# Performance work log

Hardware: AMD Instinct MI355X
Metric: run time of the kernel (lower is better)

Reference implementation:

```python
import jax, jax.numpy as jnp
import numpy as np

B, T, D = 4, 2048, 1024

def setup_inputs() -> dict:
    key = jax.random.key(0)
    kx, kq, kk, kv = jax.random.split(key, 4)
    return {
        "vector": jax.random.normal(kx, (B, T, D), dtype=jnp.float32),
        # original uses torch.rand -> uniform [0,1)
        "W_queries": jax.random.uniform(kq, (D, D), dtype=jnp.float32),
        "W_keys": jax.random.uniform(kk, (D, D), dtype=jnp.float32),
        "W_values": jax.random.uniform(kv, (D, D), dtype=jnp.float32),
    }

def reference(vector, W_queries, W_keys, W_values):
    b, num_token, d_out = vector.shape
    queries = vector @ W_queries          # [b, t, d]
    keys = vector @ W_keys                # [b, t, d]
    values = vector @ W_values            # [b, t, d]
    # attention_score: [b, q, k]
    scores = jnp.einsum('bqd,bkd->bqk', queries, keys)
    causal_mask = jnp.triu(jnp.ones((num_token, num_token), dtype=bool), k=1)
    scores = jnp.where(causal_mask[None, :, :], -jnp.inf, scores)
    # NOTE: original uses FLOOR division `//` by sqrt(d_k) -- faithful here.
    inv_sqrt_scale = jnp.asarray(np.sqrt(keys.shape[-1]), dtype=scores.dtype)
    weights = jnp.floor(scores / inv_sqrt_scale)
    # NOTE: original applies softmax over dim=1 (the query axis), not dim=-1.
    weights = jax.nn.softmax(weights, axis=1)
    # dropout rate is 0.0 (eval/deterministic): identity
    context = jnp.einsum('bqk,bkd->bqd', weights, values)
    return context
```

## Files before the change

kernel.cpp:

```cpp
#include <hip/hip_runtime.h>
#include <math.h>

typedef _Float16 half4 __attribute__((ext_vector_type(4)));
typedef _Float16 half8 __attribute__((ext_vector_type(8)));
typedef float f32x4 __attribute__((ext_vector_type(4)));

#define GLD16(gptr, lptr)                                                     \
    __builtin_amdgcn_global_load_lds(                                         \
        (const __attribute__((address_space(1))) unsigned int*)(gptr),        \
        (__attribute__((address_space(3))) unsigned int*)(lptr), 16, 0, 0)

#define WAIT_VM(N) asm volatile("s_waitcnt vmcnt(" #N ")" ::: "memory")
#define BARRIER()  __builtin_amdgcn_s_barrier()
#define SCHED_FENCE() __builtin_amdgcn_sched_barrier(0)

namespace {

constexpr int Bb = 4;
constexpr int Tt = 2048;
constexpr int Dd = 1024;
constexpr int BT = Bb * Tt;
constexpr int NCH = 16;

__device__ inline _Float16 f2h(float f) { return (_Float16)f; }

__global__ __launch_bounds__(256) void convert_x_kernel(
    const float* __restrict__ X, _Float16* __restrict__ Xhi, _Float16* __restrict__ Xlo)
{
    const int idx = (blockIdx.x * 256 + threadIdx.x) * 4;
    const float4 v = *(const float4*)(X + idx);
    const float a[4] = {v.x, v.y, v.z, v.w};
    half4 h, l;
#pragma unroll
    for (int i = 0; i < 4; ++i) {
        h[i] = f2h(a[i]);
        l[i] = f2h(a[i] - (float)h[i]);
    }
    *(half4*)(Xhi + idx) = h;
    *(half4*)(Xlo + idx) = l;
}

__global__ __launch_bounds__(256) void convert_wqk_kernel(
    const float* __restrict__ Wq, const float* __restrict__ Wk,
    _Float16* __restrict__ Wqh, _Float16* __restrict__ Wql,
    _Float16* __restrict__ Wkh, _Float16* __restrict__ Wkl)
{
    const int mat = blockIdx.y;
    const float* W = mat ? Wk : Wq;
    _Float16* Hh = mat ? Wkh : Wqh;
    _Float16* Ll = mat ? Wkl : Wql;
    const int idx = (blockIdx.x * 256 + threadIdx.x) * 4;
    const float4 v = *(const float4*)(W + idx);
    const float a[4] = {v.x, v.y, v.z, v.w};
    half4 h, l;
#pragma unroll
    for (int i = 0; i < 4; ++i) {
        h[i] = f2h(a[i]);
        l[i] = f2h(a[i] - (float)h[i]);
    }
    *(half4*)(Hh + idx) = h;
    *(half4*)(Ll + idx) = l;
}

__global__ __launch_bounds__(256) void convert_wv_kernel(
    const float* __restrict__ Wv, _Float16* __restrict__ WvTh)
{
    __shared__ float tile[64][65];
    const int n0 = blockIdx.x * 64, k0 = blockIdx.y * 64;
    const int tx = threadIdx.x & 63, ty = threadIdx.x >> 6;
#pragma unroll
    for (int i = 0; i < 16; ++i)
        tile[ty + i * 4][tx] = Wv[(size_t)(k0 + ty + i * 4) * Dd + n0 + tx];
    __syncthreads();
#pragma unroll
    for (int i = 0; i < 16; ++i) {
        const float v = tile[tx][ty + i * 4];
        WvTh[(size_t)(n0 + ty + i * 4) * Dd + k0 + tx] = f2h(v);
    }
}

__global__ __launch_bounds__(256) void gt_kernel(
    const _Float16* __restrict__ Wkh, const _Float16* __restrict__ Wkl,
    const _Float16* __restrict__ Wqh, const _Float16* __restrict__ Wql,
    _Float16* __restrict__ GTh, _Float16* __restrict__ GTl)
{
    __shared__ _Float16 Ahl[2][2][4][512];
    __shared__ _Float16 Bhl[2][2][4][512];

    const int n0 = blockIdx.x * 64;
    const int m0 = blockIdx.y * 64;
    const int tid = threadIdx.x;
    const int w = tid >> 6, lane = tid & 63;
    const int lr = lane & 15, lq = lane >> 4;
    const int wi = (w >> 1) * 2, wj = (w & 1) * 2;

    f32x4 acc[2][2];
#pragma unroll
    for (int i = 0; i < 2; ++i)
#pragma unroll
        for (int j = 0; j < 2; ++j)
#pragma unroll
            for (int c = 0; c < 4; ++c) acc[i][j][c] = 0.f;

    auto stage = [&](int bf, int kk) {
        const int s = w;
        const size_t ar = (size_t)(m0 + s * 16 + lr) * Dd + kk + lq * 8;
        const size_t br = (size_t)(n0 + s * 16 + lr) * Dd + kk + lq * 8;
        GLD16(Wkh + ar, &Ahl[bf][0][s][0]);
        GLD16(Wkl + ar, &Ahl[bf][1][s][0]);
        GLD16(Wqh + br, &Bhl[bf][0][s][0]);
        GLD16(Wql + br, &Bhl[bf][1][s][0]);
    };

    stage(0, 0);
    int ib = 0;
    for (int step = 0; step < 32; ++step, ib ^= 1) {
        if (step < 31) {
            stage(ib ^ 1, (step + 1) << 5);
            WAIT_VM(4);
        } else {
            WAIT_VM(0);
        }
        BARRIER();
        SCHED_FENCE();
        half8 ah[2], al[2], bh[2], bl[2];
#pragma unroll
        for (int i = 0; i < 2; ++i) {
            ah[i] = *(const half8*)&Ahl[ib][0][wi + i][lane * 8];
            al[i] = *(const half8*)&Ahl[ib][1][wi + i][lane * 8];
        }
#pragma unroll
        for (int j = 0; j < 2; ++j) {
            bh[j] = *(const half8*)&Bhl[ib][0][wj + j][lane * 8];
            bl[j] = *(const half8*)&Bhl[ib][1][wj + j][lane * 8];
        }
#pragma unroll
        for (int i = 0; i < 2; ++i)
#pragma unroll
            for (int j = 0; j < 2; ++j) {
                acc[i][j] = __builtin_amdgcn_mfma_f32_16x16x32_f16(ah[i], bh[j], acc[i][j], 0, 0, 0);
                acc[i][j] = __builtin_amdgcn_mfma_f32_16x16x32_f16(ah[i], bl[j], acc[i][j], 0, 0, 0);
                acc[i][j] = __builtin_amdgcn_mfma_f32_16x16x32_f16(al[i], bh[j], acc[i][j], 0, 0, 0);
            }
        BARRIER();
    }

#pragma unroll
    for (int i = 0; i < 2; ++i)
#pragma unroll
        for (int r = 0; r < 4; ++r) {
            const int row = m0 + (wi + i) * 16 + lq * 4 + r;
#pragma unroll
            for (int j = 0; j < 2; ++j) {
                const int col = n0 + (wj + j) * 16 + lr;
                const float v = acc[i][j][r];
                const _Float16 h = f2h(v);
                GTh[(size_t)row * Dd + col] = h;
                GTl[(size_t)row * Dd + col] = f2h(v - (float)h);
            }
        }
}

__global__ __launch_bounds__(256, 2) void tv_kernel(
    const _Float16* __restrict__ Xhi, const _Float16* __restrict__ Xlo,
    const _Float16* __restrict__ GTh, const _Float16* __restrict__ GTl,
    const _Float16* __restrict__ WvTh,
    _Float16* __restrict__ Thi, _Float16* __restrict__ Tlo,
    _Float16* __restrict__ Vt)
{
    __shared__ _Float16 smem[32768];
    auto A_ = [&](int bf, int hl, int s) -> _Float16* {
        return smem + ((bf * 2 + hl) * 8 + s) * 512;
    };
    auto B_ = [&](int bf, int hl, int s) -> _Float16* {
        return smem + 16384 + ((bf * 2 + hl) * 8 + s) * 512;
    };

    const int f  = blockIdx.x;
    const int fp = (f & 7) * 128 + (f >> 3);
    const int mb  = fp >> 4;
    const int sub = fp & 15;
    const int m0 = mb * 128;
    const int n0 = (sub & 7) * 128;

    const int tid = threadIdx.x;
    const int w = tid >> 6, lane = tid & 63;
    const int lr = lane & 15, lq = lane >> 4;
    const int wr = (w >> 1) * 4, wc = (w & 1) * 4;

    f32x4 acc[4][4];
#pragma unroll
    for (int i = 0; i < 4; ++i)
#pragma unroll
        for (int j = 0; j < 4; ++j)
#pragma unroll
            for (int c = 0; c < 4; ++c) acc[i][j][c] = 0.f;

    if (sub < 8) {
        auto stage = [&](int bf, int kk) {
#pragma unroll
            for (int s2 = 0; s2 < 2; ++s2) {
                const int s = w * 2 + s2;
                const size_t ar = (size_t)(m0 + s * 16 + lr) * Dd + kk + lq * 8;
                const size_t br = (size_t)(n0 + s * 16 + lr) * Dd + kk + lq * 8;
                GLD16(Xhi + ar, A_(bf, 0, s));
                GLD16(Xlo + ar, A_(bf, 1, s));
                GLD16(GTh + br, B_(bf, 0, s));
                GLD16(GTl + br, B_(bf, 1, s));
            }
        };
        stage(0, 0);
        int ib = 0;
        for (int step = 0; step < 32; ++step, ib ^= 1) {
            if (step < 31) {
                stage(ib ^ 1, (step + 1) << 5);
                WAIT_VM(8);
            } else {
                WAIT_VM(0);
            }
            BARRIER();
            SCHED_FENCE();
            half8 ah[4], al[4], bh[4], bl[4];
#pragma unroll
            for (int i = 0; i < 4; ++i) {
                ah[i] = *(const half8*)(A_(ib, 0, wr + i) + lane * 8);
                al[i] = *(const half8*)(A_(ib, 1, wr + i) + lane * 8);
            }
#pragma unroll
            for (int j = 0; j < 4; ++j) {
                bh[j] = *(const half8*)(B_(ib, 0, wc + j) + lane * 8);
                bl[j] = *(const half8*)(B_(ib, 1, wc + j) + lane * 8);
            }
#pragma unroll
            for (int i = 0; i < 4; ++i)
#pragma unroll
                for (int j = 0; j < 4; ++j) {
                    acc[i][j] = __builtin_amdgcn_mfma_f32_16x16x32_f16(ah[i], bh[j], acc[i][j], 0, 0, 0);
                    acc[i][j] = __builtin_amdgcn_mfma_f32_16x16x32_f16(ah[i], bl[j], acc[i][j], 0, 0, 0);
                    acc[i][j] = __builtin_amdgcn_mfma_f32_16x16x32_f16(al[i], bh[j], acc[i][j], 0, 0, 0);
                }
            BARRIER();
        }
#pragma unroll
        for (int i = 0; i < 4; ++i)
#pragma unroll
            for (int r = 0; r < 4; ++r) {
                const int row = m0 + (wr + i) * 16 + lq * 4 + r;
#pragma unroll
                for (int j = 0; j < 4; ++j) {
                    const int col = n0 + (wc + j) * 16 + lr;
                    const float v = acc[i][j][r];
                    const _Float16 h = f2h(v);
                    Thi[(size_t)row * Dd + col] = h;
                    Tlo[(size_t)row * Dd + col] = f2h(v - (float)h);
                }
            }
    } else {
        auto stage = [&](int bf, int kk) {
#pragma unroll
            for (int s2 = 0; s2 < 2; ++s2) {
                const int s = w * 2 + s2;
                GLD16(Xhi + (size_t)(m0 + s * 16 + lr) * Dd + kk + lq * 8, A_(bf, 0, s));
                GLD16(WvTh + (size_t)(n0 + s * 16 + lr) * Dd + kk + lq * 8, B_(bf, 0, s));
            }
        };
        stage(0, 0);
        int ib = 0;
        for (int step = 0; step < 32; ++step, ib ^= 1) {
            if (step < 31) {
                stage(ib ^ 1, (step + 1) << 5);
                WAIT_VM(4);
            } else {
                WAIT_VM(0);
            }
            BARRIER();
            SCHED_FENCE();
            half8 a[4], b2[4];
#pragma unroll
            for (int i = 0; i < 4; ++i) a[i] = *(const half8*)(A_(ib, 0, wr + i) + lane * 8);
#pragma unroll
            for (int j = 0; j < 4; ++j) b2[j] = *(const half8*)(B_(ib, 0, wc + j) + lane * 8);
#pragma unroll
            for (int i = 0; i < 4; ++i)
#pragma unroll
                for (int j = 0; j < 4; ++j)
                    acc[i][j] = __builtin_amdgcn_mfma_f32_16x16x32_f16(a[i], b2[j], acc[i][j], 0, 0, 0);
            BARRIER();
        }
        __syncthreads();
#pragma unroll
        for (int i = 0; i < 4; ++i)
#pragma unroll
            for (int r2 = 0; r2 < 4; ++r2) {
                const int rloc = (wr + i) * 16 + lq * 4 + r2;
#pragma unroll
                for (int j = 0; j < 4; ++j) {
                    const int cloc = (wc + j) * 16 + lr;
                    smem[cloc * 136 + rloc] = f2h(acc[i][j][r2]);
                }
            }
        __syncthreads();
        const int b2i = m0 >> 11;
        const int t0  = m0 & 2047;
        const int dloc = tid >> 1, tl = (tid & 1) * 64;
        _Float16* vp = Vt + (size_t)b2i * Dd * Tt + (size_t)(n0 + dloc) * Tt + t0 + tl;
#pragma unroll
        for (int e = 0; e < 8; ++e)
            *(half8*)(vp + e * 8) = *(const half8*)&smem[dloc * 136 + tl + e * 8];
    }
}

__global__ __launch_bounds__(256, 2) void scores_mfma_kernel(
    const _Float16* __restrict__ Thi, const _Float16* __restrict__ Tlo,
    const _Float16* __restrict__ Xhi, const _Float16* __restrict__ Xlo,
    float* __restrict__ S, float* __restrict__ Pm, float* __restrict__ Pl)
{
    const int f  = blockIdx.x;
    const int fp = (f & 7) * 68 + (f >> 3);
    const int b = fp / 136;
    const int t = fp - b * 136;
    int byi = (int)((sqrtf(8.f * t + 1.f) - 1.f) * 0.5f);
    if ((byi + 1) * (byi + 2) / 2 <= t) ++byi;
    if (byi * (byi + 1) / 2 > t) --byi;
    const int bxi = t - byi * (byi + 1) / 2;
    const int j0 = bxi * 128, q0 = byi * 128;
    float* Sb = S + (size_t)b * Tt * Tt;

    __shared__ _Float16 Ahl[2][2][8][512];
    __shared__ _Float16 Bhl[2][2][8][512];
    const _Float16* Th = Thi + (size_t)b * Tt * Dd;
    const _Float16* Tl = Tlo + (size_t)b * Tt * Dd;
    const _Float16* Xh = Xhi + (size_t)b * Tt * Dd;
    const _Float16* Xl = Xlo + (size_t)b * Tt * Dd;

    const int tid = threadIdx.x;
    const int w = tid >> 6, lane = tid & 63;
    const int lr = lane & 15, lq = lane >> 4;
    const int wr = (w >> 1) * 4, wc = (w & 1) * 4;

    f32x4 acc[4][4];
#pragma unroll
    for (int i = 0; i < 4; ++i)
#pragma unroll
        for (int j = 0; j < 4; ++j)
#pragma unroll
            for (int c = 0; c < 4; ++c) acc[i][j][c] = 0.f;

    auto stage = [&](int bf, int kk) {
#pragma unroll
        for (int s2 = 0; s2 < 2; ++s2) {
            const int s = w * 2 + s2;
            const size_t ar = (size_t)(q0 + s * 16 + lr) * Dd + kk + lq * 8;
            const size_t br = (size_t)(j0 + s * 16 + lr) * Dd + kk + lq * 8;
            GLD16(Th + ar, &Ahl[bf][0][s][0]);
            GLD16(Tl + ar, &Ahl[bf][1][s][0]);
            GLD16(Xh + br, &Bhl[bf][0][s][0]);
            GLD16(Xl + br, &Bhl[bf][1][s][0]);
        }
    };

    stage(0, 0);
    int ib = 0;
    for (int step = 0; step < 32; ++step, ib ^= 1) {
        if (step < 31) {
            stage(ib ^ 1, (step + 1) << 5);
            WAIT_VM(8);
        } else {
            WAIT_VM(0);
        }
        BARRIER();
        SCHED_FENCE();
        half8 ah[4], al[4], bh[4], bl[4];
#pragma unroll
        for (int i = 0; i < 4; ++i) {
            ah[i] = *(const half8*)&Ahl[ib][0][wr + i][lane * 8];
            al[i] = *(const half8*)&Ahl[ib][1][wr + i][lane * 8];
        }
#pragma unroll
        for (int j = 0; j < 4; ++j) {
            bh[j] = *(const half8*)&Bhl[ib][0][wc + j][lane * 8];
            bl[j] = *(const half8*)&Bhl[ib][1][wc + j][lane * 8];
        }
#pragma unroll
        for (int i = 0; i < 4; ++i)
#pragma unroll
            for (int j = 0; j < 4; ++j) {
                acc[i][j] = __builtin_amdgcn_mfma_f32_16x16x32_f16(ah[i], bh[j], acc[i][j], 0, 0, 0);
                acc[i][j] = __builtin_amdgcn_mfma_f32_16x16x32_f16(ah[i], bl[j], acc[i][j], 0, 0, 0);
                acc[i][j] = __builtin_amdgcn_mfma_f32_16x16x32_f16(al[i], bh[j], acc[i][j], 0, 0, 0);
            }
        BARRIER();
    }

    float sv[4][4][4];
#pragma unroll
    for (int i = 0; i < 4; ++i)
#pragma unroll
        for (int r = 0; r < 4; ++r) {
            const int q = q0 + (wr + i) * 16 + lq * 4 + r;
#pragma unroll
            for (int j = 0; j < 4; ++j) {
                const int jg = j0 + (wc + j) * 16 + lr;
                const float v = (jg <= q) ? floorf(acc[i][j][r] * 0.03125f) : -INFINITY;
                sv[i][j][r] = v;
                Sb[(size_t)q * Tt + jg] = v;
            }
        }

    float* red  = (float*)&Ahl[0][0][0][0];
    float* colm = red + 2048;
    __syncthreads();
    for (int e = tid; e < 2048; e += 256) red[e] = -INFINITY;
    __syncthreads();
    const int rowidx = (w * 4 + lq) * 128;
#pragma unroll
    for (int j = 0; j < 4; ++j) {
        const int c = (wc + j) * 16 + lr;
        float lm = -INFINITY;
#pragma unroll
        for (int i = 0; i < 4; ++i)
#pragma unroll
            for (int r = 0; r < 4; ++r) lm = fmaxf(lm, sv[i][j][r]);
        red[rowidx + c] = lm;
    }
    __syncthreads();
    if (tid < 128) {
        float m = -INFINITY;
#pragma unroll
        for (int e = 0; e < 16; ++e) m = fmaxf(m, red[e * 128 + tid]);
        colm[tid] = m;
    }
    __syncthreads();
    float ls[4];
#pragma unroll
    for (int j = 0; j < 4; ++j) {
        const int c = (wc + j) * 16 + lr;
        const float m = colm[c];
        float s = 0.f;
#pragma unroll
        for (int i = 0; i < 4; ++i)
#pragma unroll
            for (int r = 0; r < 4; ++r)
                if (sv[i][j][r] != -INFINITY) s += __expf(sv[i][j][r] - m);
        ls[j] = s;
    }
    __syncthreads();
    for (int e = tid; e < 2048; e += 256) red[e] = 0.f;
    __syncthreads();
#pragma unroll
    for (int j = 0; j < 4; ++j) red[rowidx + (wc + j) * 16 + lr] = ls[j];
    __syncthreads();
    if (tid < 128) {
        float l = 0.f;
#pragma unroll
        for (int e = 0; e < 16; ++e) l += red[e * 128 + tid];
        const size_t o = ((size_t)b * NCH + byi) * Tt + j0 + tid;
        Pm[o] = colm[tid];
        Pl[o] = l;
    }
}

__global__ __launch_bounds__(256) void colstats_merge_kernel(
    const float* __restrict__ Pm, const float* __restrict__ Pl,
    float* __restrict__ Mb, float* __restrict__ Lb)
{
    const int j = blockIdx.x * 256 + threadIdx.x;
    const int b = blockIdx.y;
    const int jt = j >> 7;
    float m = -INFINITY, l = 0.f;
    for (int c = jt; c < NCH; ++c) {
        const size_t pidx = ((size_t)b * NCH + c) * Tt + j;
        const float mi = Pm[pidx];
        if (mi == -INFINITY) continue;
        const float li = Pl[pidx];
        if (mi > m) { l = l * __expf(m - mi) + li; m = mi; }
        else        { l += li * __expf(mi - m); }
    }
    Mb[(size_t)b * Tt + j] = m;
    Lb[(size_t)b * Tt + j] = (l > 0.f) ? 1.f / l : 0.f;
}

__global__ __launch_bounds__(256) void context_mfma_kernel(
    const float* __restrict__ S, const float* __restrict__ Mb,
    const float* __restrict__ Lb, const _Float16* __restrict__ Vt,
    float* __restrict__ Out)
{
    __shared__ _Float16 As[8][512];
    __shared__ _Float16 Bl[2][8][512];

    const int f  = blockIdx.x;
    const int fp = (f & 7) * 64 + (f >> 3);
    const int b  = fp >> 7;
    const int r  = fp & 127;
    const int bx = r & 7;
    const int tq = r >> 3;
    const int by = (tq & 1) ? (15 - (tq >> 1)) : (tq >> 1);
    const int d0 = bx * 128;
    const int q0 = by * 128;
    const float* Sb = S + (size_t)b * Tt * Tt;
    const float* Mp = Mb + (size_t)b * Tt;
    const float* Lp = Lb + (size_t)b * Tt;
    const _Float16* Vb = Vt + (size_t)b * Dd * Tt;
    float* Ob = Out + (size_t)b * Tt * Dd;

    const int tid = threadIdx.x;
    const int w = tid >> 6, lane = tid & 63;
    const int lr = lane & 15, lq = lane >> 4;
    const int wr = (w >> 1) * 4, wc = (w & 1) * 4;

    f32x4 acc[4][4];
#pragma unroll
    for (int i = 0; i < 4; ++i)
#pragma unroll
        for (int j = 0; j < 4; ++j)
#pragma unroll
            for (int c = 0; c < 4; ++c) acc[i][j][c] = 0.f;

    float4 sreg[4];
    float4 mreg[2], lreg[2];

    auto issue = [&](int ib2, int k0) {
        const int kc = k0 + lq * 8;
#pragma unroll
        for (int s2 = 0; s2 < 2; ++s2) {
            const int s = w * 2 + s2;
            const float* sp = Sb + (size_t)(q0 + s * 16 + lr) * Tt + kc;
            sreg[s2 * 2]     = *(const float4*)sp;
            sreg[s2 * 2 + 1] = *(const float4*)(sp + 4);
        }
        mreg[0] = *(const float4*)(Mp + kc);
        mreg[1] = *(const float4*)(Mp + kc + 4);
        lreg[0] = *(const float4*)(Lp + kc);
        lreg[1] = *(const float4*)(Lp + kc + 4);
#pragma unroll
        for (int s2 = 0; s2 < 2; ++s2) {
            const int s = w * 2 + s2;
            GLD16(Vb + (size_t)(d0 + s * 16 + lr) * Tt + k0 + lq * 8, &Bl[ib2][s][0]);
        }
    };
    auto writeA = [&]() {
        const float mm[8] = {mreg[0].x, mreg[0].y, mreg[0].z, mreg[0].w,
                             mreg[1].x, mreg[1].y, mreg[1].z, mreg[1].w};
        const float ll[8] = {lreg[0].x, lreg[0].y, lreg[0].z, lreg[0].w,
                             lreg[1].x, lreg[1].y, lreg[1].z, lreg[1].w};
#pragma unroll
        for (int s2 = 0; s2 < 2; ++s2) {
            const int s = w * 2 + s2;
            const float4 s0 = sreg[s2 * 2], s1 = sreg[s2 * 2 + 1];
            const float sa[8] = {s0.x, s0.y, s0.z, s0.w, s1.x, s1.y, s1.z, s1.w};
            half8 out;
#pragma unroll
            for (int e = 0; e < 8; ++e)
                out[e] = f2h(__expf(sa[e] - mm[e]) * ll[e]);
            *(half8*)&As[s][lane * 8] = out;
        }
    };

    const int nstep = (q0 + 128) >> 5;
    issue(0, 0);
    writeA();
    __syncthreads();
    int ib = 0;
    for (int step = 0; step < nstep; ++step, ib ^= 1) {
        const bool more = (step + 1 < nstep);
        if (more) issue(ib ^ 1, (step + 1) << 5);
        half8 a[4], b2[4];
#pragma unroll
        for (int i = 0; i < 4; ++i) a[i] = *(const half8*)&As[wr + i][lane * 8];
#pragma unroll
        for (int j = 0; j < 4; ++j) b2[j] = *(const half8*)&Bl[ib][wc + j][lane * 8];
#pragma unroll
        for (int i = 0; i < 4; ++i)
#pragma unroll
            for (int j = 0; j < 4; ++j)
                acc[i][j] = __builtin_amdgcn_mfma_f32_16x16x32_f16(a[i], b2[j], acc[i][j], 0, 0, 0);
        if (more) {
            __syncthreads();
            writeA();
            __syncthreads();
        }
    }

#pragma unroll
    for (int i = 0; i < 4; ++i)
#pragma unroll
        for (int r2 = 0; r2 < 4; ++r2) {
            const int row = q0 + (wr + i) * 16 + lq * 4 + r2;
#pragma unroll
            for (int j = 0; j < 4; ++j)
                Ob[(size_t)row * Dd + d0 + (wc + j) * 16 + lr] = acc[i][j][r2];
        }
}

}

extern "C" void kernel_launch(void* const* d_in, const int* in_sizes, int n_in,
                              void* d_out, int out_size, void* d_ws, size_t ws_size,
                              hipStream_t stream)
{
    const float* X  = (const float*)d_in[0];
    const float* Wq = (const float*)d_in[1];
    const float* Wk = (const float*)d_in[2];
    const float* Wv = (const float*)d_in[3];

    char* ws = (char*)d_ws;
    const size_t MB = 1024 * 1024;
    _Float16* Xhi  = (_Float16*)ws;
    _Float16* Xlo  = (_Float16*)(ws + 16 * MB);
    _Float16* Wqh  = (_Float16*)(ws + 32 * MB);
    _Float16* Wql  = (_Float16*)(ws + 34 * MB);
    _Float16* Wkh  = (_Float16*)(ws + 36 * MB);
    _Float16* Wkl  = (_Float16*)(ws + 38 * MB);
    _Float16* WvTh = (_Float16*)(ws + 40 * MB);
    _Float16* GTh  = (_Float16*)(ws + 44 * MB);
    _Float16* GTl  = (_Float16*)(ws + 46 * MB);
    _Float16* Thi  = (_Float16*)(ws + 48 * MB);
    _Float16* Tlo  = (_Float16*)(ws + 64 * MB);
    _Float16* Vt   = (_Float16*)(ws + 80 * MB);
    float*    S    = (float*)(ws + 112 * MB);
    float*    Mb   = (float*)(ws + 176 * MB);
    float*    Lb   = Mb + (size_t)Bb * Tt;
    float*    Pm   = Lb + (size_t)Bb * Tt;
    float*    Pl   = Pm + (size_t)Bb * NCH * Tt;
    float*    Out  = (float*)d_out;

    convert_x_kernel<<<BT * Dd / 1024, 256, 0, stream>>>(X, Xhi, Xlo);
    convert_wqk_kernel<<<dim3(Dd * Dd / 1024, 2), 256, 0, stream>>>(Wq, Wk, Wqh, Wql, Wkh, Wkl);
    convert_wv_kernel<<<dim3(16, 16), 256, 0, stream>>>(Wv, WvTh);
    gt_kernel<<<dim3(16, 16), 256, 0, stream>>>(Wkh, Wkl, Wqh, Wql, GTh, GTl);
    tv_kernel<<<dim3(1024), 256, 0, stream>>>(Xhi, Xlo, GTh, GTl, WvTh, Thi, Tlo, Vt);
    scores_mfma_kernel<<<dim3(544), 256, 0, stream>>>(Thi, Tlo, Xhi, Xlo, S, Pm, Pl);
    colstats_merge_kernel<<<dim3(Tt / 256, Bb), 256, 0, stream>>>(Pm, Pl, Mb, Lb);
    context_mfma_kernel<<<dim3(512), 256, 0, stream>>>(S, Mb, Lb, Vt, Out);
}
```

Baseline: 469.7 us.

## Store tile-local exp probabilities as fp16 and fuse conversion kernels

The scores kernel now writes exp(s - tile column max) as fp16 instead of the raw fp32 scores. The context kernel rescales these using a per-column factor exp(Pm - M) * (1/L), precomputed into shared memory, instead of recomputing exp from fp32 scores. This halves the intermediate matrix traffic and removes exp work from the context loop. The three conversion kernels are also merged into one launch. The risk is extra fp16 rounding of the unnormalized probabilities, and the loop barrier placement changes.

```diff
diff --git a/kernel.cpp b/kernel.cpp
--- a/kernel.cpp
+++ b/kernel.cpp
@@ -24,58 +24,58 @@
 
 __device__ inline _Float16 f2h(float f) { return (_Float16)f; }
 
-__global__ __launch_bounds__(256) void convert_x_kernel(
-    const float* __restrict__ X, _Float16* __restrict__ Xhi, _Float16* __restrict__ Xlo)
-{
-    const int idx = (blockIdx.x * 256 + threadIdx.x) * 4;
-    const float4 v = *(const float4*)(X + idx);
-    const float a[4] = {v.x, v.y, v.z, v.w};
-    half4 h, l;
-#pragma unroll
-    for (int i = 0; i < 4; ++i) {
-        h[i] = f2h(a[i]);
-        l[i] = f2h(a[i] - (float)h[i]);
-    }
-    *(half4*)(Xhi + idx) = h;
-    *(half4*)(Xlo + idx) = l;
-}
-
-__global__ __launch_bounds__(256) void convert_wqk_kernel(
-    const float* __restrict__ Wq, const float* __restrict__ Wk,
+__global__ __launch_bounds__(256) void convert_all_kernel(
+    const float* __restrict__ X,  const float* __restrict__ Wq,
+    const float* __restrict__ Wk, const float* __restrict__ Wv,
+    _Float16* __restrict__ Xhi, _Float16* __restrict__ Xlo,
     _Float16* __restrict__ Wqh, _Float16* __restrict__ Wql,
-    _Float16* __restrict__ Wkh, _Float16* __restrict__ Wkl)
-{
-    const int mat = blockIdx.y;
-    const float* W = mat ? Wk : Wq;
-    _Float16* Hh = mat ? Wkh : Wqh;
-    _Float16* Ll = mat ? Wkl : Wql;
-    const int idx = (blockIdx.x * 256 + threadIdx.x) * 4;
-    const float4 v = *(const float4*)(W + idx);
-    const float a[4] = {v.x, v.y, v.z, v.w};
-    half4 h, l;
-#pragma unroll
-    for (int i = 0; i < 4; ++i) {
-        h[i] = f2h(a[i]);
-        l[i] = f2h(a[i] - (float)h[i]);
-    }
-    *(half4*)(Hh + idx) = h;
-    *(half4*)(Ll + idx) = l;
-}
-
-__global__ __launch_bounds__(256) void convert_wv_kernel(
-    const float* __restrict__ Wv, _Float16* __restrict__ WvTh)
+    _Float16* __restrict__ Wkh, _Float16* __restrict__ Wkl,
+    _Float16* __restrict__ WvTh)
 {
     __shared__ float tile[64][65];
-    const int n0 = blockIdx.x * 64, k0 = blockIdx.y * 64;
-    const int tx = threadIdx.x & 63, ty = threadIdx.x >> 6;
-#pragma unroll
-    for (int i = 0; i < 16; ++i)
-        tile[ty + i * 4][tx] = Wv[(size_t)(k0 + ty + i * 4) * Dd + n0 + tx];
-    __syncthreads();
-#pragma unroll
-    for (int i = 0; i < 16; ++i) {
-        const float v = tile[tx][ty + i * 4];
-        WvTh[(size_t)(n0 + ty + i * 4) * Dd + k0 + tx] = f2h(v);
+    const int f = blockIdx.x;
+    if (f < 8192) {
+        const int idx = f * 1024 + threadIdx.x * 4;
+        const float4 v = *(const float4*)(X + idx);
+        const float a[4] = {v.x, v.y, v.z, v.w};
+        half4 h, l;
+#pragma unroll
+        for (int i = 0; i < 4; ++i) {
+            h[i] = f2h(a[i]);
+            l[i] = f2h(a[i] - (float)h[i]);
+        }
+        *(half4*)(Xhi + idx) = h;
+        *(half4*)(Xlo + idx) = l;
+    } else if (f < 10240) {
+        const int g = f - 8192;
+        const int mat = g >> 10;
+        const float* W = mat ? Wk : Wq;
+        _Float16* Hh = mat ? Wkh : Wqh;
+        _Float16* Ll = mat ? Wkl : Wql;
+        const int idx = (g & 1023) * 1024 + threadIdx.x * 4;
+        const float4 v = *(const float4*)(W + idx);
+        const float a[4] = {v.x, v.y, v.z, v.w};
+        half4 h, l;
+#pragma unroll
+        for (int i = 0; i < 4; ++i) {
+            h[i] = f2h(a[i]);
+            l[i] = f2h(a[i] - (float)h[i]);
+        }
+        *(half4*)(Hh + idx) = h;
+        *(half4*)(Ll + idx) = l;
+    } else {
+        const int g = f - 10240;
+        const int n0 = (g & 15) * 64, k0 = (g >> 4) * 64;
+        const int tx = threadIdx.x & 63, ty = threadIdx.x >> 6;
+#pragma unroll
+        for (int i = 0; i < 16; ++i)
+            tile[ty + i * 4][tx] = Wv[(size_t)(k0 + ty + i * 4) * Dd + n0 + tx];
+        __syncthreads();
+#pragma unroll
+        for (int i = 0; i < 16; ++i) {
+            const float v = tile[tx][ty + i * 4];
+            WvTh[(size_t)(n0 + ty + i * 4) * Dd + k0 + tx] = f2h(v);
+        }
     }
 }
 
@@ -313,7 +313,7 @@
 __global__ __launch_bounds__(256, 2) void scores_mfma_kernel(
     const _Float16* __restrict__ Thi, const _Float16* __restrict__ Tlo,
     const _Float16* __restrict__ Xhi, const _Float16* __restrict__ Xlo,
-    float* __restrict__ S, float* __restrict__ Pm, float* __restrict__ Pl)
+    _Float16* __restrict__ Pp, float* __restrict__ Pm, float* __restrict__ Pl)
 {
     const int f  = blockIdx.x;
     const int fp = (f & 7) * 68 + (f >> 3);
@@ -324,7 +324,7 @@
     if (byi * (byi + 1) / 2 > t) --byi;
     const int bxi = t - byi * (byi + 1) / 2;
     const int j0 = bxi * 128, q0 = byi * 128;
-    float* Sb = S + (size_t)b * Tt * Tt;
+    _Float16* Pb = Pp + (size_t)b * Tt * Tt;
 
     __shared__ _Float16 Ahl[2][2][8][512];
     __shared__ _Float16 Bhl[2][2][8][512];
@@ -401,9 +401,7 @@
 #pragma unroll
             for (int j = 0; j < 4; ++j) {
                 const int jg = j0 + (wc + j) * 16 + lr;
-                const float v = (jg <= q) ? floorf(acc[i][j][r] * 0.03125f) : -INFINITY;
-                sv[i][j][r] = v;
-                Sb[(size_t)q * Tt + jg] = v;
+                sv[i][j][r] = (jg <= q) ? floorf(acc[i][j][r] * 0.03125f) : -INFINITY;
             }
         }
 
@@ -435,13 +433,18 @@
 #pragma unroll
     for (int j = 0; j < 4; ++j) {
         const int c = (wc + j) * 16 + lr;
+        const int jg = j0 + c;
         const float m = colm[c];
         float s = 0.f;
 #pragma unroll
         for (int i = 0; i < 4; ++i)
 #pragma unroll
-            for (int r = 0; r < 4; ++r)
-                if (sv[i][j][r] != -INFINITY) s += __expf(sv[i][j][r] - m);
+            for (int r = 0; r < 4; ++r) {
+                const float e = __expf(sv[i][j][r] - m);
+                s += e;
+                const int q = q0 + (wr + i) * 16 + lq * 4 + r;
+                Pb[(size_t)q * Tt + jg] = f2h(e);
+            }
         ls[j] = s;
     }
     __syncthreads();
@@ -481,12 +484,13 @@
 }
 
 __global__ __launch_bounds__(256) void context_mfma_kernel(
-    const float* __restrict__ S, const float* __restrict__ Mb,
-    const float* __restrict__ Lb, const _Float16* __restrict__ Vt,
-    float* __restrict__ Out)
+    const _Float16* __restrict__ Pp, const float* __restrict__ Pm,
+    const float* __restrict__ Mb, const float* __restrict__ Lb,
+    const _Float16* __restrict__ Vt, float* __restrict__ Out)
 {
     __shared__ _Float16 As[8][512];
     __shared__ _Float16 Bl[2][8][512];
+    __shared__ float cbuf[2048];
 
     const int f  = blockIdx.x;
     const int fp = (f & 7) * 64 + (f >> 3);
@@ -497,7 +501,8 @@
     const int by = (tq & 1) ? (15 - (tq >> 1)) : (tq >> 1);
     const int d0 = bx * 128;
     const int q0 = by * 128;
-    const float* Sb = S + (size_t)b * Tt * Tt;
+    const _Float16* Pb = Pp + (size_t)b * Tt * Tt;
+    const float* Pmb = Pm + ((size_t)b * NCH + by) * Tt;
     const float* Mp = Mb + (size_t)b * Tt;
     const float* Lp = Lb + (size_t)b * Tt;
     const _Float16* Vb = Vt + (size_t)b * Dd * Tt;
@@ -507,6 +512,10 @@
     const int w = tid >> 6, lane = tid & 63;
     const int lr = lane & 15, lq = lane >> 4;
     const int wr = (w >> 1) * 4, wc = (w & 1) * 4;
+    const int kmax = q0 + 128;
+
+    for (int k = tid; k < kmax; k += 256)
+        cbuf[k] = __expf(Pmb[k] - Mp[k]) * Lp[k];
 
     f32x4 acc[4][4];
 #pragma unroll
@@ -516,54 +525,50 @@
 #pragma unroll
             for (int c = 0; c < 4; ++c) acc[i][j][c] = 0.f;
 
-    float4 sreg[4];
-    float4 mreg[2], lreg[2];
-
-    auto issue = [&](int ib2, int k0) {
-        const int kc = k0 + lq * 8;
+    half8 areg[2];
+    auto loadA = [&](int k0) {
 #pragma unroll
         for (int s2 = 0; s2 < 2; ++s2) {
             const int s = w * 2 + s2;
-            const float* sp = Sb + (size_t)(q0 + s * 16 + lr) * Tt + kc;
-            sreg[s2 * 2]     = *(const float4*)sp;
-            sreg[s2 * 2 + 1] = *(const float4*)(sp + 4);
-        }
-        mreg[0] = *(const float4*)(Mp + kc);
-        mreg[1] = *(const float4*)(Mp + kc + 4);
-        lreg[0] = *(const float4*)(Lp + kc);
-        lreg[1] = *(const float4*)(Lp + kc + 4);
+            areg[s2] = *(const half8*)(Pb + (size_t)(q0 + s * 16 + lr) * Tt + k0 + lq * 8);
+        }
+    };
+    auto issueV = [&](int ib2, int k0) {
 #pragma unroll
         for (int s2 = 0; s2 < 2; ++s2) {
             const int s = w * 2 + s2;
             GLD16(Vb + (size_t)(d0 + s * 16 + lr) * Tt + k0 + lq * 8, &Bl[ib2][s][0]);
         }
     };
-    auto writeA = [&]() {
-        const float mm[8] = {mreg[0].x, mreg[0].y, mreg[0].z, mreg[0].w,
-                             mreg[1].x, mreg[1].y, mreg[1].z, mreg[1].w};
-        const float ll[8] = {lreg[0].x, lreg[0].y, lreg[0].z, lreg[0].w,
-                             lreg[1].x, lreg[1].y, lreg[1].z, lreg[1].w};
+    auto writeA = [&](int k0) {
+        const float* cp = cbuf + k0 + lq * 8;
+        float cv[8];
+#pragma unroll
+        for (int e = 0; e < 8; ++e) cv[e] = cp[e];
 #pragma unroll
         for (int s2 = 0; s2 < 2; ++s2) {
             const int s = w * 2 + s2;
-            const float4 s0 = sreg[s2 * 2], s1 = sreg[s2 * 2 + 1];
-            const float sa[8] = {s0.x, s0.y, s0.z, s0.w, s1.x, s1.y, s1.z, s1.w};
             half8 out;
 #pragma unroll
-            for (int e = 0; e < 8; ++e)
-                out[e] = f2h(__expf(sa[e] - mm[e]) * ll[e]);
+            for (int e = 0; e < 8; ++e) out[e] = f2h((float)areg[s2][e] * cv[e]);
             *(half8*)&As[s][lane * 8] = out;
         }
     };
 
-    const int nstep = (q0 + 128) >> 5;
-    issue(0, 0);
-    writeA();
-    __syncthreads();
+    __syncthreads();
+    loadA(0);
+    issueV(0, 0);
+    writeA(0);
+    __syncthreads();
+
     int ib = 0;
+    const int nstep = kmax >> 5;
     for (int step = 0; step < nstep; ++step, ib ^= 1) {
         const bool more = (step + 1 < nstep);
-        if (more) issue(ib ^ 1, (step + 1) << 5);
+        if (more) {
+            loadA((step + 1) << 5);
+            issueV(ib ^ 1, (step + 1) << 5);
+        }
         half8 a[4], b2[4];
 #pragma unroll
         for (int i = 0; i < 4; ++i) a[i] = *(const half8*)&As[wr + i][lane * 8];
@@ -574,9 +579,10 @@
 #pragma unroll
             for (int j = 0; j < 4; ++j)
                 acc[i][j] = __builtin_amdgcn_mfma_f32_16x16x32_f16(a[i], b2[j], acc[i][j], 0, 0, 0);
+        BARRIER();
+        SCHED_FENCE();
         if (more) {
-            __syncthreads();
-            writeA();
+            writeA((step + 1) << 5);
             __syncthreads();
         }
     }
@@ -617,19 +623,18 @@
     _Float16* Thi  = (_Float16*)(ws + 48 * MB);
     _Float16* Tlo  = (_Float16*)(ws + 64 * MB);
     _Float16* Vt   = (_Float16*)(ws + 80 * MB);
-    float*    S    = (float*)(ws + 112 * MB);
+    _Float16* Pp   = (_Float16*)(ws + 112 * MB);
     float*    Mb   = (float*)(ws + 176 * MB);
     float*    Lb   = Mb + (size_t)Bb * Tt;
     float*    Pm   = Lb + (size_t)Bb * Tt;
     float*    Pl   = Pm + (size_t)Bb * NCH * Tt;
     float*    Out  = (float*)d_out;
 
-    convert_x_kernel<<<BT * Dd / 1024, 256, 0, stream>>>(X, Xhi, Xlo);
-    convert_wqk_kernel<<<dim3(Dd * Dd / 1024, 2), 256, 0, stream>>>(Wq, Wk, Wqh, Wql, Wkh, Wkl);
-    convert_wv_kernel<<<dim3(16, 16), 256, 0, stream>>>(Wv, WvTh);
+    convert_all_kernel<<<10496, 256, 0, stream>>>(X, Wq, Wk, Wv, Xhi, Xlo,
+                                                  Wqh, Wql, Wkh, Wkl, WvTh);
     gt_kernel<<<dim3(16, 16), 256, 0, stream>>>(Wkh, Wkl, Wqh, Wql, GTh, GTl);
     tv_kernel<<<dim3(1024), 256, 0, stream>>>(Xhi, Xlo, GTh, GTl, WvTh, Thi, Tlo, Vt);
-    scores_mfma_kernel<<<dim3(544), 256, 0, stream>>>(Thi, Tlo, Xhi, Xlo, S, Pm, Pl);
+    scores_mfma_kernel<<<dim3(544), 256, 0, stream>>>(Thi, Tlo, Xhi, Xlo, Pp, Pm, Pl);
     colstats_merge_kernel<<<dim3(Tt / 256, Bb), 256, 0, stream>>>(Pm, Pl, Mb, Lb);
-    context_mfma_kernel<<<dim3(512), 256, 0, stream>>>(S, Mb, Lb, Vt, Out);
-}
+    context_mfma_kernel<<<dim3(512), 256, 0, stream>>>(Pp, Pm, Mb, Lb, Vt, Out);
+}
```

New measurement: 440.9 us. 6.1% less time.
